# Kernel tuning notes

Measured on AMD Instinct MI355X. Metric: run time of the kernel, lower is better.

The kernel has to match this reference:

```python
import jax, jax.numpy as jnp
import numpy as np

POOL_SIZES = (1, 3, 6, 8)
EPS = 1e-5


def conv1x1(x, W, b):
    # x: [b, cin, h, w], W: [cout, cin], b: [cout]
    return jnp.einsum('bchw,oc->bohw', x, W) + b[None, :, None, None]


def ppm(x):
    # x: [b, c, h, w] -> [b, c, S] with S = sum(p*p); H,W divisible by each p
    b, c, h, w = x.shape
    outs = []
    for p in POOL_SIZES:
        pooled = x.reshape(b, c, p, h // p, p, w // p).mean(axis=(3, 5))
        outs.append(pooled.reshape(b, c, p * p))
    return jnp.concatenate(outs, axis=-1)


def setup_inputs() -> dict:
    key = jax.random.key(0)
    ks = jax.random.split(key, 8)
    B, Cin, H, W = 4, 512, 120, 120
    Ck, Cv, Cout = 256, 256, 512
    x = jax.random.normal(ks[0], (B, Cin, H, W), dtype=jnp.float32)
    sc = lambda cin: 1.0 / np.sqrt(cin)
    Wk = jax.random.normal(ks[1], (Ck, Cin), dtype=jnp.float32) * sc(Cin)
    bk = jnp.zeros((Ck,), jnp.float32)
    gamma = jnp.ones((Ck,), jnp.float32)
    beta = jnp.zeros((Ck,), jnp.float32)
    mean = jax.random.normal(ks[2], (Ck,), dtype=jnp.float32) * 0.1
    var = jax.random.uniform(ks[3], (Ck,), dtype=jnp.float32, minval=0.5, maxval=1.5)
    Wv = jax.random.normal(ks[4], (Cv, Cin), dtype=jnp.float32) * sc(Cin)
    bv = jnp.zeros((Cv,), jnp.float32)
    # original inits Conv_Out to zero; use random weights for a nontrivial baseline
    Wo = jax.random.normal(ks[5], (Cout, Cv), dtype=jnp.float32) * sc(Cv)
    bo = jnp.zeros((Cout,), jnp.float32)
    return {'x': x, 'Wk': Wk, 'bk': bk, 'gamma': gamma, 'beta': beta,
            'mean': mean, 'var': var, 'Wv': Wv, 'bv': bv, 'Wo': Wo, 'bo': bo}


def reference(x, Wk, bk, gamma, beta, mean, var, Wv, bv, Wo, bo):
    b, _, h, w = x.shape
    ck = Wk.shape[0]
    cv = Wv.shape[0]
    # shared Conv_Key / Conv_Query: conv1x1 -> BN (inference) -> ReLU
    kq = conv1x1(x, Wk, bk)
    inv = gamma / jnp.sqrt(var + EPS)
    kq = jax.nn.relu(kq * inv[None, :, None, None] + (beta - mean * inv)[None, :, None, None])
    value = ppm(conv1x1(x, Wv, bv)).transpose(0, 2, 1)      # [b, S, cv]
    key = ppm(kq)                                            # [b, ck, S]
    query = kq.reshape(b, ck, h * w).transpose(0, 2, 1)      # [b, hw, ck]
    scores = jnp.einsum('bnc,bcs->bns', query, key) * (ck ** -0.5)
    attn = jax.nn.softmax(scores, axis=-1)                   # [b, hw, S]
    agg = jnp.einsum('bns,bsv->bnv', attn, value)            # [b, hw, cv]
    agg = agg.transpose(0, 2, 1).reshape(b, cv, h, w)
    return conv1x1(agg, Wo, bo)
```

## Files before the change

kernel.cpp:

```cpp
#include <hip/hip_runtime.h>
#include <cstdint>
#include <cstddef>

#define HW 14400
#define WIDTH 120
#define S_TOT 110

typedef unsigned short u16;
typedef __attribute__((ext_vector_type(8))) short bf16x8;
typedef __attribute__((ext_vector_type(4))) float f32x4;

__device__ __forceinline__ u16 f2bf(float x) {
  unsigned u = __float_as_uint(x);
  unsigned r = (u + 0x7fffu + ((u >> 16) & 1u)) >> 16;
  return (u16)r;
}
__device__ __forceinline__ float bf2f(u16 h) {
  return __uint_as_float((unsigned)h << 16);
}

__device__ __forceinline__ void async16(void* lds, const void* g) {
  __builtin_amdgcn_global_load_lds(
      (const __attribute__((address_space(1))) void*)g,
      (__attribute__((address_space(3))) void*)lds, 16, 0, 0);
}

__global__ __launch_bounds__(256) void pool_kernel(const float* __restrict__ in,
                                                   float* __restrict__ outp) {
  __shared__ float part[576];
  const float* plane = in + (size_t)blockIdx.x * HW;
  int t = threadIdx.x;
  for (int bb = t; bb < 576; bb += 256) {
    int by = bb / 24, bx = bb % 24;
    const float* p0 = plane + (by * 5) * WIDTH + bx * 5;
    float s = 0.f;
#pragma unroll
    for (int yy = 0; yy < 5; ++yy)
#pragma unroll
      for (int xx = 0; xx < 5; ++xx) s += p0[yy * WIDTH + xx];
    part[bb] = s;
  }
  __syncthreads();
  if (t < S_TOT) {
    float s = 0.f;
    if (t == 0) {
      for (int i = 0; i < 576; ++i) s += part[i];
      s *= (1.f / 14400.f);
    } else if (t < 10) {
      int idx = t - 1, i = idx / 3, j = idx % 3;
      for (int a = 0; a < 8; ++a)
        for (int c = 0; c < 8; ++c) s += part[(i * 8 + a) * 24 + (j * 8 + c)];
      s *= (1.f / 1600.f);
    } else if (t < 46) {
      int idx = t - 10, i = idx / 6, j = idx % 6;
      for (int a = 0; a < 4; ++a)
        for (int c = 0; c < 4; ++c) s += part[(i * 4 + a) * 24 + (j * 4 + c)];
      s *= (1.f / 400.f);
    } else {
      int idx = t - 46, i = idx / 8, j = idx % 8;
      for (int a = 0; a < 3; ++a)
        for (int c = 0; c < 3; ++c) s += part[(i * 3 + a) * 24 + (j * 3 + c)];
      s *= (1.f / 225.f);
    }
    outp[(size_t)blockIdx.x * S_TOT + t] = s;
  }
}

__global__ __launch_bounds__(256) void convert_w(const float* __restrict__ in,
                                                 u16* __restrict__ hi,
                                                 u16* __restrict__ lo, int n) {
  int i = blockIdx.x * 256 + threadIdx.x;
  if (i < n) {
    float v = in[i];
    u16 h = f2bf(v);
    hi[i] = h;
    lo[i] = f2bf(v - bf2f(h));
  }
}

template <int CIN>
__global__ __launch_bounds__(256) void convert_t(const float* __restrict__ X,
                                                 u16* __restrict__ xth,
                                                 u16* __restrict__ xtl) {
  __shared__ float ls[64][65];
  int b = blockIdx.z;
  int n0 = blockIdx.x * 64, k0 = blockIdx.y * 64;
  int t = threadIdx.x;
  int rt = t >> 4, c4 = (t & 15) * 4;
#pragma unroll
  for (int rr = 0; rr < 4; ++rr) {
    int kk = rr * 16 + rt;
    float4 v = *(const float4*)&X[((size_t)(b * CIN + k0 + kk)) * HW + n0 + c4];
    ls[kk][c4] = v.x; ls[kk][c4 + 1] = v.y; ls[kk][c4 + 2] = v.z; ls[kk][c4 + 3] = v.w;
  }
  __syncthreads();
#pragma unroll
  for (int rr = 0; rr < 4; ++rr) {
    int nn = rr * 16 + rt;
    float v0 = ls[c4 + 0][nn], v1 = ls[c4 + 1][nn], v2 = ls[c4 + 2][nn], v3 = ls[c4 + 3][nn];
    ushort4 oh, ol;
    oh.x = f2bf(v0); ol.x = f2bf(v0 - bf2f(oh.x));
    oh.y = f2bf(v1); ol.y = f2bf(v1 - bf2f(oh.y));
    oh.z = f2bf(v2); ol.z = f2bf(v2 - bf2f(oh.z));
    oh.w = f2bf(v3); ol.w = f2bf(v3 - bf2f(oh.w));
    size_t idx = ((size_t)(b * HW + n0 + nn)) * CIN + k0 + c4;
    *(ushort4*)&xth[idx] = oh;
    *(ushort4*)&xtl[idx] = ol;
  }
}

template <int K, int M_TOT, bool BNRELU>
__global__ __launch_bounds__(256) void gemm_mfma(
    const u16* __restrict__ Ah, const u16* __restrict__ Al,
    const u16* __restrict__ Bh, const u16* __restrict__ Bl,
    float* __restrict__ C,
    const float* __restrict__ p0, const float* __restrict__ p1,
    const float* __restrict__ p2, const float* __restrict__ p3,
    const float* __restrict__ p4) {
  constexpr int NSTEP = K / 32;
  __shared__ alignas(16) u16 sAh[256 * 32];
  __shared__ alignas(16) u16 sAl[256 * 32];
  __shared__ alignas(16) u16 sBh[64 * 32];
  __shared__ alignas(16) u16 sBl[64 * 32];
  __shared__ float sP0[256], sP1[256];

  int t = threadIdx.x, w = t >> 6, l = t & 63;
  int b = blockIdx.z;
  int n0 = blockIdx.x * 64;
  int m0 = blockIdx.y * 256;

  if (BNRELU) {
    int m = m0 + t;
    float iv = p1[m] * rsqrtf(p4[m] + 1e-5f);
    sP0[t] = iv;
    sP1[t] = (p0[m] - p3[m]) * iv + p2[m];
  } else {
    sP0[t] = p0[m0 + t];
  }

  int crow = l >> 2;
  int cbyte = (l & 3) * 16;
  const size_t bOff = (size_t)b * HW;

  f32x4 acc[4][4];
#pragma unroll
  for (int i = 0; i < 4; ++i)
#pragma unroll
    for (int j = 0; j < 4; ++j) acc[i][j] = (f32x4){0.f, 0.f, 0.f, 0.f};

  int fr = l & 15, fk = (l >> 4) * 8;

  for (int ks = 0; ks < NSTEP; ++ks) {
    int k0 = ks * 32;
#pragma unroll
    for (int c = 0; c < 10; ++c) {
      int i = w * 10 + c;
      const u16* g;
      u16* d;
      if (i < 16) {
        g = Ah + (size_t)(m0 + i * 16 + crow) * K + k0;
        d = sAh + i * 512;
      } else if (i < 32) {
        g = Al + (size_t)(m0 + (i - 16) * 16 + crow) * K + k0;
        d = sAl + (i - 16) * 512;
      } else if (i < 36) {
        g = Bh + (bOff + n0 + (i - 32) * 16 + crow) * K + k0;
        d = sBh + (i - 32) * 512;
      } else {
        g = Bl + (bOff + n0 + (i - 36) * 16 + crow) * K + k0;
        d = sBl + (i - 36) * 512;
      }
      async16((char*)d, (const char*)g + cbyte);
    }
    __syncthreads();

    bf16x8 ah[4], al[4], bh[4], bl[4];
#pragma unroll
    for (int mt = 0; mt < 4; ++mt) {
      int r = w * 64 + mt * 16 + fr;
      ah[mt] = *(const bf16x8*)&sAh[r * 32 + fk];
      al[mt] = *(const bf16x8*)&sAl[r * 32 + fk];
    }
#pragma unroll
    for (int nt = 0; nt < 4; ++nt) {
      int r = nt * 16 + fr;
      bh[nt] = *(const bf16x8*)&sBh[r * 32 + fk];
      bl[nt] = *(const bf16x8*)&sBl[r * 32 + fk];
    }
#pragma unroll
    for (int mt = 0; mt < 4; ++mt)
#pragma unroll
      for (int nt = 0; nt < 4; ++nt) {
        acc[mt][nt] = __builtin_amdgcn_mfma_f32_16x16x32_bf16(ah[mt], bh[nt], acc[mt][nt], 0, 0, 0);
        acc[mt][nt] = __builtin_amdgcn_mfma_f32_16x16x32_bf16(ah[mt], bl[nt], acc[mt][nt], 0, 0, 0);
        acc[mt][nt] = __builtin_amdgcn_mfma_f32_16x16x32_bf16(al[mt], bh[nt], acc[mt][nt], 0, 0, 0);
      }
    __syncthreads();
  }

#pragma unroll
  for (int mt = 0; mt < 4; ++mt) {
    int lmBase = w * 64 + mt * 16 + (l >> 4) * 4;
#pragma unroll
    for (int nt = 0; nt < 4; ++nt) {
      int n = n0 + nt * 16 + fr;
#pragma unroll
      for (int r = 0; r < 4; ++r) {
        int lm = lmBase + r;
        float v = acc[mt][nt][r];
        if (BNRELU)
          v = fmaxf(v * sP0[lm] + sP1[lm], 0.f);
        else
          v = v + sP0[lm];
        C[((size_t)(b * M_TOT + m0 + lm)) * HW + n] = v;
      }
    }
  }
}

__global__ __launch_bounds__(256) void value_kernel(
    const float* __restrict__ Wv, const float* __restrict__ xp,
    const float* __restrict__ bv, u16* __restrict__ vth,
    u16* __restrict__ vtl) {
  int b = blockIdx.x >> 7, s = blockIdx.x & 127;
  int t = threadIdx.x;
  size_t o = ((size_t)(b * 256 + t)) * 128 + s;
  if (s >= S_TOT) { vth[o] = 0; vtl[o] = 0; return; }
  __shared__ float xs[512];
  for (int i = t; i < 512; i += 256) xs[i] = xp[((size_t)b * 512 + i) * S_TOT + s];
  __syncthreads();
  float accv = 0.f;
  const float* wv = Wv + (size_t)t * 512;
  for (int k = 0; k < 512; k += 4) {
    float4 w4 = *(const float4*)&wv[k];
    accv += w4.x * xs[k] + w4.y * xs[k + 1] + w4.z * xs[k + 2] + w4.w * xs[k + 3];
  }
  accv += bv[t];
  u16 h = f2bf(accv);
  vth[o] = h;
  vtl[o] = f2bf(accv - bf2f(h));
}

__global__ __launch_bounds__(256) void convert_key(const float* __restrict__ keyp,
                                                   u16* __restrict__ kth,
                                                   u16* __restrict__ ktl) {
  int b = blockIdx.x;
  int t = threadIdx.x;
  for (int i = t; i < 128 * 256; i += 256) {
    int s = i >> 8, c = i & 255;
    float v = (s < S_TOT) ? keyp[((size_t)(b * 256 + c)) * S_TOT + s] : 0.f;
    u16 h = f2bf(v);
    size_t o = ((size_t)(b * 128 + s)) * 256 + c;
    kth[o] = h;
    ktl[o] = f2bf(v - bf2f(h));
  }
}

__global__ __launch_bounds__(256) void attn_mfma(
    const u16* __restrict__ qh, const u16* __restrict__ ql,
    const u16* __restrict__ kh, const u16* __restrict__ kl,
    const u16* __restrict__ vh, const u16* __restrict__ vl,
    u16* __restrict__ aggh, u16* __restrict__ aggl) {
  __shared__ alignas(16) u16 lds[17408];
  int b = blockIdx.y, pix0 = blockIdx.x * 64;
  int t = threadIdx.x, w = t >> 6, l = t & 63;
  int fr = l & 15, q = l >> 4;

  const u16* kbase_h = kh + (size_t)b * 128 * 256;
  const u16* kbase_l = kl + (size_t)b * 128 * 256;

  f32x4 acc[8];
#pragma unroll
  for (int st = 0; st < 8; ++st) acc[st] = (f32x4){0.f, 0.f, 0.f, 0.f};

  const u16* qbh = qh + ((size_t)(b * HW + pix0 + w * 16 + fr)) * 256 + q * 8;
  const u16* qbl = ql + ((size_t)(b * HW + pix0 + w * 16 + fr)) * 256 + q * 8;

  auto stageK = [&](int ks, int buf) {
    int c0 = ks * 32;
#pragma unroll
    for (int j = 0; j < 4; ++j) {
      int i = t + j * 256;
      int half = i >> 9;
      int idx = i & 511;
      int st = idx >> 6, ll = idx & 63;
      const u16* src = (half ? kbase_l : kbase_h) +
                       (st * 16 + (ll & 15)) * 256 + c0 + (ll >> 4) * 8;
      async16(&lds[buf * 8192 + half * 4096 + idx * 8], src);
    }
  };

  stageK(0, 0);
  for (int ks = 0; ks < 8; ++ks) {
    __syncthreads();
    if (ks < 7) stageK(ks + 1, (ks + 1) & 1);
    bf16x8 ah = *(const bf16x8*)(qbh + ks * 32);
    bf16x8 al = *(const bf16x8*)(qbl + ks * 32);
    const u16* kb = &lds[(ks & 1) * 8192 + l * 8];
#pragma unroll
    for (int st = 0; st < 8; ++st) {
      bf16x8 bh = *(const bf16x8*)(kb + st * 512);
      bf16x8 bl = *(const bf16x8*)(kb + 4096 + st * 512);
      acc[st] = __builtin_amdgcn_mfma_f32_16x16x32_bf16(ah, bh, acc[st], 0, 0, 0);
      acc[st] = __builtin_amdgcn_mfma_f32_16x16x32_bf16(ah, bl, acc[st], 0, 0, 0);
      acc[st] = __builtin_amdgcn_mfma_f32_16x16x32_bf16(al, bh, acc[st], 0, 0, 0);
    }
  }

#pragma unroll
  for (int st = 0; st < 8; ++st)
#pragma unroll
    for (int r = 0; r < 4; ++r) acc[st][r] *= 0.0625f;
  if (fr >= 14) {
#pragma unroll
    for (int r = 0; r < 4; ++r) acc[6][r] = -1e30f;
  }
#pragma unroll
  for (int r = 0; r < 4; ++r) acc[7][r] = -1e30f;

#pragma unroll
  for (int r = 0; r < 4; ++r) {
    float m = -1e30f;
#pragma unroll
    for (int st = 0; st < 8; ++st) m = fmaxf(m, acc[st][r]);
    m = fmaxf(m, __shfl_xor(m, 1));
    m = fmaxf(m, __shfl_xor(m, 2));
    m = fmaxf(m, __shfl_xor(m, 4));
    m = fmaxf(m, __shfl_xor(m, 8));
    float s = 0.f;
#pragma unroll
    for (int st = 0; st < 8; ++st) {
      float e = __expf(acc[st][r] - m);
      acc[st][r] = e;
      s += e;
    }
    s += __shfl_xor(s, 1);
    s += __shfl_xor(s, 2);
    s += __shfl_xor(s, 4);
    s += __shfl_xor(s, 8);
    float inv = 1.f / s;
#pragma unroll
    for (int st = 0; st < 8; ++st) acc[st][r] *= inv;
  }

  __syncthreads();

  int prow = w * 16 + q * 4;
#pragma unroll
  for (int st = 0; st < 8; ++st) {
    int s = st * 16 + fr;
#pragma unroll
    for (int r = 0; r < 4; ++r) {
      float v = acc[st][r];
      u16 h = f2bf(v);
      lds[(prow + r) * 136 + s] = h;
      lds[8704 + (prow + r) * 136 + s] = f2bf(v - bf2f(h));
    }
  }
  __syncthreads();

  f32x4 oacc[4][4];
#pragma unroll
  for (int nt = 0; nt < 4; ++nt)
#pragma unroll
    for (int pt = 0; pt < 4; ++pt) oacc[nt][pt] = (f32x4){0.f, 0.f, 0.f, 0.f};

  const u16* vbh = vh + ((size_t)(b * 256 + w * 64 + fr)) * 128 + q * 8;
  const u16* vbl = vl + ((size_t)(b * 256 + w * 64 + fr)) * 128 + q * 8;

#pragma unroll
  for (int kc = 0; kc < 4; ++kc) {
    bf16x8 ph[4], pl[4];
#pragma unroll
    for (int pt = 0; pt < 4; ++pt) {
      ph[pt] = *(const bf16x8*)&lds[(pt * 16 + fr) * 136 + kc * 32 + q * 8];
      pl[pt] = *(const bf16x8*)&lds[8704 + (pt * 16 + fr) * 136 + kc * 32 + q * 8];
    }
#pragma unroll
    for (int nt = 0; nt < 4; ++nt) {
      bf16x8 a_h = *(const bf16x8*)(vbh + (size_t)nt * 16 * 128 + kc * 32);
      bf16x8 a_l = *(const bf16x8*)(vbl + (size_t)nt * 16 * 128 + kc * 32);
#pragma unroll
      for (int pt = 0; pt < 4; ++pt) {
        oacc[nt][pt] = __builtin_amdgcn_mfma_f32_16x16x32_bf16(a_h, ph[pt], oacc[nt][pt], 0, 0, 0);
        oacc[nt][pt] = __builtin_amdgcn_mfma_f32_16x16x32_bf16(a_h, pl[pt], oacc[nt][pt], 0, 0, 0);
        oacc[nt][pt] = __builtin_amdgcn_mfma_f32_16x16x32_bf16(a_l, ph[pt], oacc[nt][pt], 0, 0, 0);
      }
    }
  }

#pragma unroll
  for (int nt = 0; nt < 4; ++nt) {
#pragma unroll
    for (int pt = 0; pt < 4; ++pt) {
      ushort4 oh, ol;
      float v0 = oacc[nt][pt][0], v1 = oacc[nt][pt][1];
      float v2 = oacc[nt][pt][2], v3 = oacc[nt][pt][3];
      oh.x = f2bf(v0); ol.x = f2bf(v0 - bf2f(oh.x));
      oh.y = f2bf(v1); ol.y = f2bf(v1 - bf2f(oh.y));
      oh.z = f2bf(v2); ol.z = f2bf(v2 - bf2f(oh.z));
      oh.w = f2bf(v3); ol.w = f2bf(v3 - bf2f(oh.w));
      size_t o = ((size_t)(b * HW + pix0 + pt * 16 + fr)) * 256 + (w * 4 + nt) * 16 + q * 4;
      *(ushort4*)&aggh[o] = oh;
      *(ushort4*)&aggl[o] = ol;
    }
  }
}

extern "C" void kernel_launch(void* const* d_in, const int* in_sizes, int n_in,
                              void* d_out, int out_size, void* d_ws, size_t ws_size,
                              hipStream_t stream) {
  (void)in_sizes; (void)n_in; (void)out_size; (void)ws_size;
  const float* x     = (const float*)d_in[0];
  const float* Wk    = (const float*)d_in[1];
  const float* bk    = (const float*)d_in[2];
  const float* gamma = (const float*)d_in[3];
  const float* beta  = (const float*)d_in[4];
  const float* mean  = (const float*)d_in[5];
  const float* var   = (const float*)d_in[6];
  const float* Wv    = (const float*)d_in[7];
  const float* bv    = (const float*)d_in[8];
  const float* Wo    = (const float*)d_in[9];
  const float* bo    = (const float*)d_in[10];
  float* out = (float*)d_out;

  char* p = (char*)d_ws;
  float* kq = (float*)p;      p += (size_t)14745600 * 4;
  u16* xth = (u16*)p;         p += (size_t)29491200 * 2;
  u16* xtl = (u16*)p;         p += (size_t)29491200 * 2;
  u16* wkh = (u16*)p;         p += 131072 * 2;
  u16* wkl = (u16*)p;         p += 131072 * 2;
  u16* woh = (u16*)p;         p += 131072 * 2;
  u16* wol = (u16*)p;         p += 131072 * 2;
  float* xp = (float*)p;      p += (size_t)4 * 512 * 110 * 4;
  float* keyp = (float*)p;    p += (size_t)4 * 256 * 110 * 4;
  u16* vth = (u16*)p;         p += (size_t)4 * 256 * 128 * 2;
  u16* vtl = (u16*)p;         p += (size_t)4 * 256 * 128 * 2;
  u16* kth = (u16*)p;         p += (size_t)4 * 128 * 256 * 2;
  u16* ktl = (u16*)p;         p += (size_t)4 * 128 * 256 * 2;
  u16* aggh = xth;
  u16* kqth = xth + (size_t)14745600;
  u16* aggl = xtl;
  u16* kqtl = xtl + (size_t)14745600;

  convert_w<<<512, 256, 0, stream>>>(Wk, wkh, wkl, 256 * 512);
  convert_w<<<512, 256, 0, stream>>>(Wo, woh, wol, 512 * 256);
  convert_t<512><<<dim3(225, 8, 4), 256, 0, stream>>>(x, xth, xtl);
  pool_kernel<<<dim3(4 * 512), dim3(256), 0, stream>>>(x, xp);
  value_kernel<<<dim3(4 * 128), dim3(256), 0, stream>>>(Wv, xp, bv, vth, vtl);
  gemm_mfma<512, 256, true><<<dim3(225, 1, 4), 256, 0, stream>>>(
      wkh, wkl, xth, xtl, kq, bk, gamma, beta, mean, var);
  convert_t<256><<<dim3(225, 4, 4), 256, 0, stream>>>(kq, kqth, kqtl);
  pool_kernel<<<dim3(4 * 256), dim3(256), 0, stream>>>(kq, keyp);
  convert_key<<<dim3(4), dim3(256), 0, stream>>>(keyp, kth, ktl);
  attn_mfma<<<dim3(225, 4), 256, 0, stream>>>(kqth, kqtl, kth, ktl, vth, vtl,
                                              aggh, aggl);
  gemm_mfma<256, 512, false><<<dim3(225, 2, 4), 256, 0, stream>>>(
      woh, wol, aggh, aggl, out, bo, nullptr, nullptr, nullptr, nullptr);
}
```

Measured before the change: 547.6 us.

## Fuse kq bf16 split-transpose into key GEMM epilogue and double-buffer B tiles

The key GEMM epilogue now also writes the transposed hi/lo bf16 split of kq whenever the workspace has room. This drops the separate convert_t launch that re-read kq. The GEMM mainloop loads A fragments straight from global memory instead of staging them in LDS, and double-buffers only the B tile with one barrier per k-step. The cost is uncoalesced 16-byte per-lane A loads with no LDS reuse across waves, plus extra epilogue register pressure.

Result: slower. 601.8 us (+9.9%).

```diff
diff --git a/kernel.cpp b/kernel.cpp
--- a/kernel.cpp
+++ b/kernel.cpp
@@ -116,12 +116,10 @@
     float* __restrict__ C,
     const float* __restrict__ p0, const float* __restrict__ p1,
     const float* __restrict__ p2, const float* __restrict__ p3,
-    const float* __restrict__ p4) {
+    const float* __restrict__ p4,
+    u16* __restrict__ Th, u16* __restrict__ Tl) {
   constexpr int NSTEP = K / 32;
-  __shared__ alignas(16) u16 sAh[256 * 32];
-  __shared__ alignas(16) u16 sAl[256 * 32];
-  __shared__ alignas(16) u16 sBh[64 * 32];
-  __shared__ alignas(16) u16 sBl[64 * 32];
+  __shared__ alignas(16) u16 sB[2][2][4][64][8];
   __shared__ float sP0[256], sP1[256];
 
   int t = threadIdx.x, w = t >> 6, l = t & 63;
@@ -138,54 +136,46 @@
     sP0[t] = p0[m0 + t];
   }
 
-  int crow = l >> 2;
-  int cbyte = (l & 3) * 16;
+  int fr = l & 15, fkc = l >> 4;
   const size_t bOff = (size_t)b * HW;
 
+  auto stageB = [&](int ks, int buf) {
+    int k0 = ks * 32;
+#pragma unroll
+    for (int c = 0; c < 2; ++c) {
+      int i = w * 2 + c;
+      int half = i >> 2, nt = i & 3;
+      const u16* src = (half ? Bl : Bh) +
+                       (bOff + n0 + nt * 16 + fr) * (size_t)K + k0 + fkc * 8;
+      async16(&sB[buf][half][nt][l][0], src);
+    }
+  };
+
   f32x4 acc[4][4];
 #pragma unroll
   for (int i = 0; i < 4; ++i)
 #pragma unroll
     for (int j = 0; j < 4; ++j) acc[i][j] = (f32x4){0.f, 0.f, 0.f, 0.f};
 
-  int fr = l & 15, fk = (l >> 4) * 8;
+  const u16* aRow_h = Ah + (size_t)(m0 + w * 64 + fr) * K + fkc * 8;
+  const u16* aRow_l = Al + (size_t)(m0 + w * 64 + fr) * K + fkc * 8;
+
+  stageB(0, 0);
 
   for (int ks = 0; ks < NSTEP; ++ks) {
-    int k0 = ks * 32;
-#pragma unroll
-    for (int c = 0; c < 10; ++c) {
-      int i = w * 10 + c;
-      const u16* g;
-      u16* d;
-      if (i < 16) {
-        g = Ah + (size_t)(m0 + i * 16 + crow) * K + k0;
-        d = sAh + i * 512;
-      } else if (i < 32) {
-        g = Al + (size_t)(m0 + (i - 16) * 16 + crow) * K + k0;
-        d = sAl + (i - 16) * 512;
-      } else if (i < 36) {
-        g = Bh + (bOff + n0 + (i - 32) * 16 + crow) * K + k0;
-        d = sBh + (i - 32) * 512;
-      } else {
-        g = Bl + (bOff + n0 + (i - 36) * 16 + crow) * K + k0;
-        d = sBl + (i - 36) * 512;
-      }
-      async16((char*)d, (const char*)g + cbyte);
-    }
     __syncthreads();
-
-    bf16x8 ah[4], al[4], bh[4], bl[4];
+    bf16x8 ah[4], al[4];
 #pragma unroll
     for (int mt = 0; mt < 4; ++mt) {
-      int r = w * 64 + mt * 16 + fr;
-      ah[mt] = *(const bf16x8*)&sAh[r * 32 + fk];
-      al[mt] = *(const bf16x8*)&sAl[r * 32 + fk];
-    }
+      ah[mt] = *(const bf16x8*)(aRow_h + (size_t)mt * 16 * K + ks * 32);
+      al[mt] = *(const bf16x8*)(aRow_l + (size_t)mt * 16 * K + ks * 32);
+    }
+    if (ks + 1 < NSTEP) stageB(ks + 1, (ks + 1) & 1);
+    bf16x8 bh[4], bl[4];
 #pragma unroll
     for (int nt = 0; nt < 4; ++nt) {
-      int r = nt * 16 + fr;
-      bh[nt] = *(const bf16x8*)&sBh[r * 32 + fk];
-      bl[nt] = *(const bf16x8*)&sBl[r * 32 + fk];
+      bh[nt] = *(const bf16x8*)&sB[ks & 1][0][nt][l][0];
+      bl[nt] = *(const bf16x8*)&sB[ks & 1][1][nt][l][0];
     }
 #pragma unroll
     for (int mt = 0; mt < 4; ++mt)
@@ -195,7 +185,6 @@
         acc[mt][nt] = __builtin_amdgcn_mfma_f32_16x16x32_bf16(ah[mt], bl[nt], acc[mt][nt], 0, 0, 0);
         acc[mt][nt] = __builtin_amdgcn_mfma_f32_16x16x32_bf16(al[mt], bh[nt], acc[mt][nt], 0, 0, 0);
       }
-    __syncthreads();
   }
 
 #pragma unroll
@@ -204,15 +193,31 @@
 #pragma unroll
     for (int nt = 0; nt < 4; ++nt) {
       int n = n0 + nt * 16 + fr;
-#pragma unroll
-      for (int r = 0; r < 4; ++r) {
-        int lm = lmBase + r;
-        float v = acc[mt][nt][r];
-        if (BNRELU)
-          v = fmaxf(v * sP0[lm] + sP1[lm], 0.f);
-        else
-          v = v + sP0[lm];
-        C[((size_t)(b * M_TOT + m0 + lm)) * HW + n] = v;
+      if (BNRELU) {
+        float v0 = fmaxf(acc[mt][nt][0] * sP0[lmBase + 0] + sP1[lmBase + 0], 0.f);
+        float v1 = fmaxf(acc[mt][nt][1] * sP0[lmBase + 1] + sP1[lmBase + 1], 0.f);
+        float v2 = fmaxf(acc[mt][nt][2] * sP0[lmBase + 2] + sP1[lmBase + 2], 0.f);
+        float v3 = fmaxf(acc[mt][nt][3] * sP0[lmBase + 3] + sP1[lmBase + 3], 0.f);
+        C[((size_t)(b * M_TOT + m0 + lmBase + 0)) * HW + n] = v0;
+        C[((size_t)(b * M_TOT + m0 + lmBase + 1)) * HW + n] = v1;
+        C[((size_t)(b * M_TOT + m0 + lmBase + 2)) * HW + n] = v2;
+        C[((size_t)(b * M_TOT + m0 + lmBase + 3)) * HW + n] = v3;
+        if (Th) {
+          ushort4 oh, ol;
+          oh.x = f2bf(v0); ol.x = f2bf(v0 - bf2f(oh.x));
+          oh.y = f2bf(v1); ol.y = f2bf(v1 - bf2f(oh.y));
+          oh.z = f2bf(v2); ol.z = f2bf(v2 - bf2f(oh.z));
+          oh.w = f2bf(v3); ol.w = f2bf(v3 - bf2f(oh.w));
+          size_t o = (bOff + n) * (size_t)M_TOT + m0 + lmBase;
+          *(ushort4*)&Th[o] = oh;
+          *(ushort4*)&Tl[o] = ol;
+        }
+      } else {
+#pragma unroll
+        for (int r = 0; r < 4; ++r) {
+          int lm = lmBase + r;
+          C[((size_t)(b * M_TOT + m0 + lm)) * HW + n] = acc[mt][nt][r] + sP0[lm];
+        }
       }
     }
   }
@@ -410,7 +415,7 @@
 extern "C" void kernel_launch(void* const* d_in, const int* in_sizes, int n_in,
                               void* d_out, int out_size, void* d_ws, size_t ws_size,
                               hipStream_t stream) {
-  (void)in_sizes; (void)n_in; (void)out_size; (void)ws_size;
+  (void)in_sizes; (void)n_in; (void)out_size;
   const float* x     = (const float*)d_in[0];
   const float* Wk    = (const float*)d_in[1];
   const float* bk    = (const float*)d_in[2];
@@ -438,10 +443,14 @@
   u16* vtl = (u16*)p;         p += (size_t)4 * 256 * 128 * 2;
   u16* kth = (u16*)p;         p += (size_t)4 * 128 * 256 * 2;
   u16* ktl = (u16*)p;         p += (size_t)4 * 128 * 256 * 2;
+  u16* kqth_f = (u16*)p;      p += (size_t)14745600 * 2;
+  u16* kqtl_f = (u16*)p;      p += (size_t)14745600 * 2;
+  bool fused = ((size_t)(p - (char*)d_ws) <= ws_size);
+
   u16* aggh = xth;
-  u16* kqth = xth + (size_t)14745600;
   u16* aggl = xtl;
-  u16* kqtl = xtl + (size_t)14745600;
+  u16* kqth = fused ? kqth_f : xth + (size_t)14745600;
+  u16* kqtl = fused ? kqtl_f : xtl + (size_t)14745600;
 
   convert_w<<<512, 256, 0, stream>>>(Wk, wkh, wkl, 256 * 512);
   convert_w<<<512, 256, 0, stream>>>(Wo, woh, wol, 512 * 256);
@@ -449,12 +458,15 @@
   pool_kernel<<<dim3(4 * 512), dim3(256), 0, stream>>>(x, xp);
   value_kernel<<<dim3(4 * 128), dim3(256), 0, stream>>>(Wv, xp, bv, vth, vtl);
   gemm_mfma<512, 256, true><<<dim3(225, 1, 4), 256, 0, stream>>>(
-      wkh, wkl, xth, xtl, kq, bk, gamma, beta, mean, var);
-  convert_t<256><<<dim3(225, 4, 4), 256, 0, stream>>>(kq, kqth, kqtl);
+      wkh, wkl, xth, xtl, kq, bk, gamma, beta, mean, var,
+      fused ? kqth : (u16*)nullptr, fused ? kqtl : (u16*)nullptr);
+  if (!fused)
+    convert_t<256><<<dim3(225, 4, 4), 256, 0, stream>>>(kq, kqth, kqtl);
   pool_kernel<<<dim3(4 * 256), dim3(256), 0, stream>>>(kq, keyp);
   convert_key<<<dim3(4), dim3(256), 0, stream>>>(keyp, kth, ktl);
   attn_mfma<<<dim3(225, 4), 256, 0, stream>>>(kqth, kqtl, kth, ktl, vth, vtl,
                                               aggh, aggl);
   gemm_mfma<256, 512, false><<<dim3(225, 2, 4), 256, 0, stream>>>(
-      woh, wol, aggh, aggl, out, bo, nullptr, nullptr, nullptr, nullptr);
-}
+      woh, wol, aggh, aggl, out, bo, nullptr, nullptr, nullptr, nullptr,
+      nullptr, nullptr);
+}
```

## Double-buffer GEMM LDS tiles and lay them out in fragment order

Applied to the files above, without the earlier changes.

The MFMA GEMM now keeps two LDS buffers, so the async global-to-LDS loads for the next K step are issued while the current step computes, with one barrier per step instead of two. The tiles are stored in MFMA fragment order, so each lane reads one contiguous 16-byte chunk and LDS bank conflicts should drop. The BN/bias parameters move out of shared memory into per-lane float4 loads in the epilogue, and a minimum of 2 blocks per CU is requested. LDS use doubles, which may limit occupancy, and the launch bound may constrain registers for the 64 accumulators.

Measured after the change: 578.9 us. 5.7% more time.

```diff
diff --git a/kernel.cpp b/kernel.cpp
--- a/kernel.cpp
+++ b/kernel.cpp
@@ -110,7 +110,7 @@
 }
 
 template <int K, int M_TOT, bool BNRELU>
-__global__ __launch_bounds__(256) void gemm_mfma(
+__global__ __launch_bounds__(256, 2) void gemm_mfma(
     const u16* __restrict__ Ah, const u16* __restrict__ Al,
     const u16* __restrict__ Bh, const u16* __restrict__ Bl,
     float* __restrict__ C,
@@ -118,39 +118,18 @@
     const float* __restrict__ p2, const float* __restrict__ p3,
     const float* __restrict__ p4) {
   constexpr int NSTEP = K / 32;
-  __shared__ alignas(16) u16 sAh[256 * 32];
-  __shared__ alignas(16) u16 sAl[256 * 32];
-  __shared__ alignas(16) u16 sBh[64 * 32];
-  __shared__ alignas(16) u16 sBl[64 * 32];
-  __shared__ float sP0[256], sP1[256];
+  __shared__ alignas(16) u16 sA[2][32][512];
+  __shared__ alignas(16) u16 sB[2][8][512];
 
   int t = threadIdx.x, w = t >> 6, l = t & 63;
   int b = blockIdx.z;
   int n0 = blockIdx.x * 64;
   int m0 = blockIdx.y * 256;
 
-  if (BNRELU) {
-    int m = m0 + t;
-    float iv = p1[m] * rsqrtf(p4[m] + 1e-5f);
-    sP0[t] = iv;
-    sP1[t] = (p0[m] - p3[m]) * iv + p2[m];
-  } else {
-    sP0[t] = p0[m0 + t];
-  }
-
-  int crow = l >> 2;
-  int cbyte = (l & 3) * 16;
+  int fr = l & 15, fkc = l >> 4;
   const size_t bOff = (size_t)b * HW;
 
-  f32x4 acc[4][4];
-#pragma unroll
-  for (int i = 0; i < 4; ++i)
-#pragma unroll
-    for (int j = 0; j < 4; ++j) acc[i][j] = (f32x4){0.f, 0.f, 0.f, 0.f};
-
-  int fr = l & 15, fk = (l >> 4) * 8;
-
-  for (int ks = 0; ks < NSTEP; ++ks) {
+  auto stage = [&](int ks, int buf) {
     int k0 = ks * 32;
 #pragma unroll
     for (int c = 0; c < 10; ++c) {
@@ -158,34 +137,44 @@
       const u16* g;
       u16* d;
       if (i < 16) {
-        g = Ah + (size_t)(m0 + i * 16 + crow) * K + k0;
-        d = sAh + i * 512;
+        g = Ah + (size_t)(m0 + i * 16 + fr) * K + k0 + fkc * 8;
+        d = &sA[buf][i][0];
       } else if (i < 32) {
-        g = Al + (size_t)(m0 + (i - 16) * 16 + crow) * K + k0;
-        d = sAl + (i - 16) * 512;
+        g = Al + (size_t)(m0 + (i - 16) * 16 + fr) * K + k0 + fkc * 8;
+        d = &sA[buf][i][0];
       } else if (i < 36) {
-        g = Bh + (bOff + n0 + (i - 32) * 16 + crow) * K + k0;
-        d = sBh + (i - 32) * 512;
+        g = Bh + (bOff + n0 + (i - 32) * 16 + fr) * (size_t)K + k0 + fkc * 8;
+        d = &sB[buf][i - 32][0];
       } else {
-        g = Bl + (bOff + n0 + (i - 36) * 16 + crow) * K + k0;
-        d = sBl + (i - 36) * 512;
+        g = Bl + (bOff + n0 + (i - 36) * 16 + fr) * (size_t)K + k0 + fkc * 8;
+        d = &sB[buf][i - 32][0];
       }
-      async16((char*)d, (const char*)g + cbyte);
-    }
+      async16(d, g);
+    }
+  };
+
+  f32x4 acc[4][4];
+#pragma unroll
+  for (int i = 0; i < 4; ++i)
+#pragma unroll
+    for (int j = 0; j < 4; ++j) acc[i][j] = (f32x4){0.f, 0.f, 0.f, 0.f};
+
+  stage(0, 0);
+
+  for (int ks = 0; ks < NSTEP; ++ks) {
     __syncthreads();
-
+    if (ks + 1 < NSTEP) stage(ks + 1, (ks + 1) & 1);
+    int cur = ks & 1;
     bf16x8 ah[4], al[4], bh[4], bl[4];
 #pragma unroll
     for (int mt = 0; mt < 4; ++mt) {
-      int r = w * 64 + mt * 16 + fr;
-      ah[mt] = *(const bf16x8*)&sAh[r * 32 + fk];
-      al[mt] = *(const bf16x8*)&sAl[r * 32 + fk];
+      ah[mt] = *(const bf16x8*)&sA[cur][w * 4 + mt][l * 8];
+      al[mt] = *(const bf16x8*)&sA[cur][16 + w * 4 + mt][l * 8];
     }
 #pragma unroll
     for (int nt = 0; nt < 4; ++nt) {
-      int r = nt * 16 + fr;
-      bh[nt] = *(const bf16x8*)&sBh[r * 32 + fk];
-      bl[nt] = *(const bf16x8*)&sBl[r * 32 + fk];
+      bh[nt] = *(const bf16x8*)&sB[cur][nt][l * 8];
+      bl[nt] = *(const bf16x8*)&sB[cur][4 + nt][l * 8];
     }
 #pragma unroll
     for (int mt = 0; mt < 4; ++mt)
@@ -195,24 +184,41 @@
         acc[mt][nt] = __builtin_amdgcn_mfma_f32_16x16x32_bf16(ah[mt], bl[nt], acc[mt][nt], 0, 0, 0);
         acc[mt][nt] = __builtin_amdgcn_mfma_f32_16x16x32_bf16(al[mt], bh[nt], acc[mt][nt], 0, 0, 0);
       }
-    __syncthreads();
   }
 
 #pragma unroll
   for (int mt = 0; mt < 4; ++mt) {
-    int lmBase = w * 64 + mt * 16 + (l >> 4) * 4;
+    int mb = m0 + w * 64 + mt * 16 + (l >> 4) * 4;
+    float iv[4], ad[4];
+    if (BNRELU) {
+      float4 g0 = *(const float4*)&p0[mb];
+      float4 g1 = *(const float4*)&p1[mb];
+      float4 g2 = *(const float4*)&p2[mb];
+      float4 g3 = *(const float4*)&p3[mb];
+      float4 g4 = *(const float4*)&p4[mb];
+      iv[0] = g1.x * rsqrtf(g4.x + 1e-5f);
+      iv[1] = g1.y * rsqrtf(g4.y + 1e-5f);
+      iv[2] = g1.z * rsqrtf(g4.z + 1e-5f);
+      iv[3] = g1.w * rsqrtf(g4.w + 1e-5f);
+      ad[0] = (g0.x - g3.x) * iv[0] + g2.x;
+      ad[1] = (g0.y - g3.y) * iv[1] + g2.y;
+      ad[2] = (g0.z - g3.z) * iv[2] + g2.z;
+      ad[3] = (g0.w - g3.w) * iv[3] + g2.w;
+    } else {
+      float4 g0 = *(const float4*)&p0[mb];
+      ad[0] = g0.x; ad[1] = g0.y; ad[2] = g0.z; ad[3] = g0.w;
+    }
 #pragma unroll
     for (int nt = 0; nt < 4; ++nt) {
       int n = n0 + nt * 16 + fr;
 #pragma unroll
       for (int r = 0; r < 4; ++r) {
-        int lm = lmBase + r;
         float v = acc[mt][nt][r];
         if (BNRELU)
-          v = fmaxf(v * sP0[lm] + sP1[lm], 0.f);
+          v = fmaxf(v * iv[r] + ad[r], 0.f);
         else
-          v = v + sP0[lm];
-        C[((size_t)(b * M_TOT + m0 + lm)) * HW + n] = v;
+          v = v + ad[r];
+        C[((size_t)(b * M_TOT) + mb + r) * HW + n] = v;
       }
     }
   }
```
